# Optimization experiments

Measured on AMD Instinct MI355X. Metric: run time of the kernel, lower is better.

The kernel has to match this reference:

```python
import jax, jax.numpy as jnp
import numpy as np


def setup_inputs() -> dict:
    key = jax.random.key(0)
    k1, k2, k3 = jax.random.split(key, 3)
    B, N, F = 32, 1024, 128
    x = jax.random.normal(k1, (B, N, F), dtype=jnp.float32)
    adj = jax.random.uniform(k2, (B, N, N), dtype=jnp.float32)
    # Linear(in_feature=128, out_feature=128) params (Kaiming-ish scale)
    W = jax.random.normal(k3, (F, F), dtype=jnp.float32) * (1.0 / np.sqrt(F))
    b = jnp.zeros((F,), dtype=jnp.float32)
    return {"x": x, "adj": adj, "W": W, "b": b}


def reference(x, adj, W, b):
    # h = W(x) ; dropout is identity in inference mode
    h = jnp.einsum("bnf,fg->bng", x, W) + b          # [B,N,F]
    h = jnp.einsum("bnm,bmf->bnf", adj, h)           # neighbor aggregation
    return jax.nn.relu(h + x)                          # residual + ReLU
```

## Files before the change

kernel.cpp:

```cpp
#include <hip/hip_runtime.h>
#include <stdint.h>

typedef unsigned short u16;
typedef __attribute__((ext_vector_type(4))) u16    u16x4;
typedef __attribute__((ext_vector_type(8))) u16    u16x8;
typedef __attribute__((ext_vector_type(4))) float  f32x4;
typedef __attribute__((ext_vector_type(8))) __bf16 bf16x8;

__device__ __forceinline__ u16 f2bf(float f) {
    union { float f; uint32_t u; } v; v.f = f;
    uint32_t u = v.u;
    uint32_t rb = 0x7FFFu + ((u >> 16) & 1u);
    return (u16)((u + rb) >> 16);
}

__global__ __launch_bounds__(256) void gcn_wt(const float* __restrict__ W,
                                              u16* __restrict__ Wt) {
    int idx = blockIdx.x * 256 + threadIdx.x;
    int k = idx >> 7, f = idx & 127;
    Wt[f * 128 + k] = f2bf(W[idx]);
}

__global__ __launch_bounds__(512, 4) void gcn_fused(const float* __restrict__ adj,
                                                    const float* __restrict__ x,
                                                    const u16* __restrict__ Wt,
                                                    const float* __restrict__ bias,
                                                    float* __restrict__ out) {
    __shared__ u16   Al[2][64 * 64];
    __shared__ u16   Xt[2][128 * 72];
    __shared__ u16   Yl[64 * 128];
    __shared__ float Rs[64];

    const int t = threadIdx.x;
    const int L  = (blockIdx.x & 7) * 64 + (blockIdx.x >> 3);
    const int bb = L >> 4;
    const int r0 = (L & 15) << 6;

    const float* adjb = adj + (size_t)bb * 1048576 + (size_t)r0 * 1024;
    const float* xb   = x + (size_t)bb * 131072;

    const int w = t >> 6, l = t & 63;
    const int wr = w >> 1, wc = w & 1;

    const int rA = t >> 3, k8 = t & 7;
    const float* gA = adjb + (size_t)rA * 1024 + k8 * 8;
    const int ldsA = rA * 128 + ((k8 * 16) ^ ((rA & 7) << 4));

    const float* gX = xb + (size_t)wr * 128 + wc * 64 + l;
    const int xWb = (wc * 64 + l) * 144 + 2 * wr;

    float rsum = 0.0f;

#define LOADT(ar, xr, ks)                                       \
    do {                                                        \
        const int n0_ = (ks) * 64;                              \
        ar[0] = *(const f32x4*)(gA + n0_);                      \
        ar[1] = *(const f32x4*)(gA + n0_ + 4);                  \
        _Pragma("unroll")                                       \
        for (int i = 0; i < 16; ++i)                            \
            xr[i] = gX[(size_t)n0_ * 128 + i * 512];            \
    } while (0)

#define WRITET(buf, ar, xr)                                     \
    do {                                                        \
        u16x8 ha;                                               \
        ha[0] = f2bf(ar[0].x); ha[1] = f2bf(ar[0].y);           \
        ha[2] = f2bf(ar[0].z); ha[3] = f2bf(ar[0].w);           \
        ha[4] = f2bf(ar[1].x); ha[5] = f2bf(ar[1].y);           \
        ha[6] = f2bf(ar[1].z); ha[7] = f2bf(ar[1].w);           \
        *(u16x8*)((char*)&Al[buf][0] + ldsA) = ha;              \
        rsum += ar[0].x + ar[0].y + ar[0].z + ar[0].w           \
              + ar[1].x + ar[1].y + ar[1].z + ar[1].w;          \
        _Pragma("unroll")                                       \
        for (int i = 0; i < 16; ++i)                            \
            *(u16*)((char*)&Xt[buf][0] + xWb + i * 8) = f2bf(xr[i]); \
    } while (0)

#define BARRIER() asm volatile("s_waitcnt lgkmcnt(0)\ns_barrier" ::: "memory")

#define COMPUTE(buf)                                                            \
    do {                                                                        \
        _Pragma("unroll")                                                       \
        for (int kk = 0; kk < 2; ++kk) {                                        \
            const int kbyteA = kk * 64 + (l >> 4) * 16;                         \
            const int rl = wr * 16 + (l & 15);                                  \
            bf16x8 a = *(const bf16x8*)((const char*)&Al[buf][0] + rl * 128 +   \
                                        (kbyteA ^ ((rl & 7) << 4)));            \
            bf16x8 b[4];                                                        \
            _Pragma("unroll")                                                   \
            for (int nn = 0; nn < 4; ++nn) {                                    \
                int fm = wc * 64 + nn * 16 + (l & 15);                          \
                b[nn] = *(const bf16x8*)((const char*)&Xt[buf][0] + fm * 144 +  \
                                         kk * 64 + (l >> 4) * 16);              \
            }                                                                   \
            _Pragma("unroll")                                                   \
            for (int nn = 0; nn < 4; ++nn)                                      \
                acc[nn] = __builtin_amdgcn_mfma_f32_16x16x32_bf16(              \
                    a, b[nn], acc[nn], 0, 0, 0);                                \
        }                                                                       \
    } while (0)

    f32x4 acc[4] = {};
    f32x4 a0[2], a1[2];
    float xs0[16], xs1[16];

    LOADT(a0, xs0, 0);
    LOADT(a1, xs1, 1);
#pragma unroll
    for (int ks = 0; ks < 16; ks += 2) {
        WRITET(0, a0, xs0);
        BARRIER();
        if (ks + 2 < 16) LOADT(a0, xs0, ks + 2);
        COMPUTE(0);
        WRITET(1, a1, xs1);
        BARRIER();
        if (ks + 3 < 16) LOADT(a1, xs1, ks + 3);
        COMPUTE(1);
    }
#undef LOADT
#undef WRITET
#undef BARRIER
#undef COMPUTE

    rsum += __shfl_xor(rsum, 1);
    rsum += __shfl_xor(rsum, 2);
    rsum += __shfl_xor(rsum, 4);
    if ((t & 7) == 0) Rs[rA] = rsum;

#pragma unroll
    for (int nn = 0; nn < 4; ++nn)
#pragma unroll
        for (int j = 0; j < 4; ++j) {
            int r = wr * 16 + (l >> 4) * 4 + j;
            int c = wc * 64 + nn * 16 + (l & 15);
            *(u16*)((char*)Yl + r * 256 + ((c * 2) ^ ((r & 7) << 4))) =
                f2bf(acc[nn][j]);
        }
    __syncthreads();

    f32x4 z[4] = {};
    const int rl2 = wr * 16 + (l & 15);
#pragma unroll
    for (int kk = 0; kk < 4; ++kk) {
        const int kbyte = kk * 64 + (l >> 4) * 16;
        bf16x8 a = *(const bf16x8*)((const char*)Yl + rl2 * 256 +
                                    (kbyte ^ ((rl2 & 7) << 4)));
#pragma unroll
        for (int nn = 0; nn < 4; ++nn) {
            int f = wc * 64 + nn * 16 + (l & 15);
            int k = kk * 32 + (l >> 4) * 8;
            bf16x8 b = *(const bf16x8*)(Wt + (size_t)f * 128 + k);
            z[nn] = __builtin_amdgcn_mfma_f32_16x16x32_bf16(a, b, z[nn], 0, 0, 0);
        }
    }

    float* ob = out + (size_t)bb * 131072;
#pragma unroll
    for (int nn = 0; nn < 4; ++nn) {
        int f = wc * 64 + nn * 16 + (l & 15);
        float bv = bias[f];
#pragma unroll
        for (int j = 0; j < 4; ++j) {
            int r = wr * 16 + (l >> 4) * 4 + j;
            size_t idx = (size_t)(r0 + r) * 128 + f;
            float v = z[nn][j] + Rs[r] * bv + xb[idx];
            ob[idx] = fmaxf(v, 0.0f);
        }
    }
}

extern "C" void kernel_launch(void* const* d_in, const int* in_sizes, int n_in,
                              void* d_out, int out_size, void* d_ws, size_t ws_size,
                              hipStream_t stream) {
    const float* x    = (const float*)d_in[0];
    const float* adj  = (const float*)d_in[1];
    const float* W    = (const float*)d_in[2];
    const float* bias = (const float*)d_in[3];
    float* out = (float*)d_out;

    u16* Wt = (u16*)d_ws;

    gcn_wt   <<<dim3(64),  dim3(256), 0, stream>>>(W, Wt);
    gcn_fused<<<dim3(512), dim3(512), 0, stream>>>(adj, x, Wt, bias, out);
}
```

Measured before the change: 49.71 us.

## Compute h=xW+b per K-tile inside the main loop, single kernel launch

Replaces the (adj·x)·W ordering with adj·(xW+b): each K-chunk of x is first multiplied by register-resident W fragments (bias folded into the accumulator init), then fed as the B operand of the adj MFMA. This removes the separate W transpose kernel, the row-sum reduction and the second post-loop GEMM through LDS, and reads the residual from the LDS x tile instead of reloading it from global. The cost is recomputing xW per block (16x redundant across row blocks), more MFMA work per K step and extra bf16 rounding of the intermediate h and of the residual x.

After: 42.32 us. 14.9% less time.

```diff
diff --git a/kernel.cpp b/kernel.cpp
--- a/kernel.cpp
+++ b/kernel.cpp
@@ -7,6 +7,9 @@
 typedef __attribute__((ext_vector_type(4))) float  f32x4;
 typedef __attribute__((ext_vector_type(8))) __bf16 bf16x8;
 
+union BF8 { u16x8 u; bf16x8 b; };
+union BF4x2 { struct { u16x4 lo, hi; } p; bf16x8 b; };
+
 __device__ __forceinline__ u16 f2bf(float f) {
     union { float f; uint32_t u; } v; v.f = f;
     uint32_t u = v.u;
@@ -14,159 +17,172 @@
     return (u16)((u + rb) >> 16);
 }
 
-__global__ __launch_bounds__(256) void gcn_wt(const float* __restrict__ W,
-                                              u16* __restrict__ Wt) {
-    int idx = blockIdx.x * 256 + threadIdx.x;
-    int k = idx >> 7, f = idx & 127;
-    Wt[f * 128 + k] = f2bf(W[idx]);
-}
-
-__global__ __launch_bounds__(512, 4) void gcn_fused(const float* __restrict__ adj,
-                                                    const float* __restrict__ x,
-                                                    const u16* __restrict__ Wt,
-                                                    const float* __restrict__ bias,
-                                                    float* __restrict__ out) {
-    __shared__ u16   Al[2][64 * 64];
-    __shared__ u16   Xt[2][128 * 72];
-    __shared__ u16   Yl[64 * 128];
-    __shared__ float Rs[64];
+__global__ __launch_bounds__(512, 4) void gcn_one(const float* __restrict__ adj,
+                                                  const float* __restrict__ x,
+                                                  const float* __restrict__ W,
+                                                  const float* __restrict__ bias,
+                                                  float* __restrict__ out) {
+    __shared__ u16 Al[2][64 * 64];
+    __shared__ u16 Xl[2][64 * 128];
+    __shared__ u16 Xr[64 * 128];
 
     const int t = threadIdx.x;
-    const int L  = (blockIdx.x & 7) * 64 + (blockIdx.x >> 3);
+    const int L = (blockIdx.x & 7) * 64 + (blockIdx.x >> 3);
     const int bb = L >> 4;
-    const int r0 = (L & 15) << 6;
+    const int myblk = L & 15;
+    const int r0 = myblk << 6;
 
     const float* adjb = adj + (size_t)bb * 1048576 + (size_t)r0 * 1024;
     const float* xb   = x + (size_t)bb * 131072;
 
     const int w = t >> 6, l = t & 63;
-    const int wr = w >> 1, wc = w & 1;
+    const int lg = l >> 4, lc = l & 15;
+    const int f = w * 16 + lc;
 
-    const int rA = t >> 3, k8 = t & 7;
-    const float* gA = adjb + (size_t)rA * 1024 + k8 * 8;
-    const int ldsA = rA * 128 + ((k8 * 16) ^ ((rA & 7) << 4));
+    const float bv = bias[f];
+    BF8 wf[4];
+#pragma unroll
+    for (int gs = 0; gs < 4; ++gs)
+#pragma unroll
+        for (int j = 0; j < 8; ++j)
+            wf[gs].b[j] = (__bf16)W[(size_t)(gs * 32 + lg * 8 + j) * 128 + f];
 
-    const float* gX = xb + (size_t)wr * 128 + wc * 64 + l;
-    const int xWb = (wc * 64 + l) * 144 + 2 * wr;
+    const int rA0 = t >> 4;
+    const int rA1 = rA0 + 32;
+    const int aOff = (t & 15) * 8;
+    const int ldsA0 = rA0 * 128 + (aOff ^ (((rA0 & 7) << 4) | (rA0 & 8)));
+    const int ldsA1 = rA1 * 128 + (aOff ^ (((rA1 & 7) << 4) | (rA1 & 8)));
+    const float* gA0 = adjb + (size_t)rA0 * 1024 + (t & 15) * 4;
+    const float* gA1 = adjb + (size_t)rA1 * 1024 + (t & 15) * 4;
 
-    float rsum = 0.0f;
+    const int xOff = (t & 31) * 8;
+    int ldsX[4];
+    const float* gX[4];
+#pragma unroll
+    for (int i = 0; i < 4; ++i) {
+        int n = (t >> 5) + i * 16;
+        ldsX[i] = n * 256 + (xOff ^ ((n & 7) << 4));
+        gX[i] = xb + (size_t)n * 128 + (t & 31) * 4;
+    }
 
-#define LOADT(ar, xr, ks)                                       \
-    do {                                                        \
-        const int n0_ = (ks) * 64;                              \
-        ar[0] = *(const f32x4*)(gA + n0_);                      \
-        ar[1] = *(const f32x4*)(gA + n0_ + 4);                  \
-        _Pragma("unroll")                                       \
-        for (int i = 0; i < 16; ++i)                            \
-            xr[i] = gX[(size_t)n0_ * 128 + i * 512];            \
+#define LOADT(ar, xr, ks)                                         \
+    do {                                                          \
+        ar[0] = *(const f32x4*)(gA0 + (ks) * 64);                 \
+        ar[1] = *(const f32x4*)(gA1 + (ks) * 64);                 \
+        _Pragma("unroll")                                         \
+        for (int i = 0; i < 4; ++i)                               \
+            xr[i] = *(const f32x4*)(gX[i] + (size_t)(ks) * 8192); \
     } while (0)
 
-#define WRITET(buf, ar, xr)                                     \
-    do {                                                        \
-        u16x8 ha;                                               \
-        ha[0] = f2bf(ar[0].x); ha[1] = f2bf(ar[0].y);           \
-        ha[2] = f2bf(ar[0].z); ha[3] = f2bf(ar[0].w);           \
-        ha[4] = f2bf(ar[1].x); ha[5] = f2bf(ar[1].y);           \
-        ha[6] = f2bf(ar[1].z); ha[7] = f2bf(ar[1].w);           \
-        *(u16x8*)((char*)&Al[buf][0] + ldsA) = ha;              \
-        rsum += ar[0].x + ar[0].y + ar[0].z + ar[0].w           \
-              + ar[1].x + ar[1].y + ar[1].z + ar[1].w;          \
-        _Pragma("unroll")                                       \
-        for (int i = 0; i < 16; ++i)                            \
-            *(u16*)((char*)&Xt[buf][0] + xWb + i * 8) = f2bf(xr[i]); \
+#define WRITET(buf, ar, xr)                                              \
+    do {                                                                 \
+        u16x4 h0, h1;                                                    \
+        h0.x = f2bf(ar[0].x); h0.y = f2bf(ar[0].y);                      \
+        h0.z = f2bf(ar[0].z); h0.w = f2bf(ar[0].w);                      \
+        h1.x = f2bf(ar[1].x); h1.y = f2bf(ar[1].y);                      \
+        h1.z = f2bf(ar[1].z); h1.w = f2bf(ar[1].w);                      \
+        *(u16x4*)((char*)&Al[buf][0] + ldsA0) = h0;                      \
+        *(u16x4*)((char*)&Al[buf][0] + ldsA1) = h1;                      \
+        _Pragma("unroll")                                                \
+        for (int i = 0; i < 4; ++i) {                                    \
+            u16x4 hx;                                                    \
+            hx.x = f2bf(xr[i].x); hx.y = f2bf(xr[i].y);                  \
+            hx.z = f2bf(xr[i].z); hx.w = f2bf(xr[i].w);                  \
+            *(u16x4*)((char*)&Xl[buf][0] + ldsX[i]) = hx;                \
+        }                                                                \
     } while (0)
 
 #define BARRIER() asm volatile("s_waitcnt lgkmcnt(0)\ns_barrier" ::: "memory")
 
-#define COMPUTE(buf)                                                            \
-    do {                                                                        \
-        _Pragma("unroll")                                                       \
-        for (int kk = 0; kk < 2; ++kk) {                                        \
-            const int kbyteA = kk * 64 + (l >> 4) * 16;                         \
-            const int rl = wr * 16 + (l & 15);                                  \
-            bf16x8 a = *(const bf16x8*)((const char*)&Al[buf][0] + rl * 128 +   \
-                                        (kbyteA ^ ((rl & 7) << 4)));            \
-            bf16x8 b[4];                                                        \
-            _Pragma("unroll")                                                   \
-            for (int nn = 0; nn < 4; ++nn) {                                    \
-                int fm = wc * 64 + nn * 16 + (l & 15);                          \
-                b[nn] = *(const bf16x8*)((const char*)&Xt[buf][0] + fm * 144 +  \
-                                         kk * 64 + (l >> 4) * 16);              \
-            }                                                                   \
-            _Pragma("unroll")                                                   \
-            for (int nn = 0; nn < 4; ++nn)                                      \
-                acc[nn] = __builtin_amdgcn_mfma_f32_16x16x32_bf16(              \
-                    a, b[nn], acc[nn], 0, 0, 0);                                \
-        }                                                                       \
+#define COPYRESID(buf)                                                        \
+    do {                                                                      \
+        u16x8 c0 = *(const u16x8*)((const char*)&Xl[buf][0] + t * 32);        \
+        u16x8 c1 = *(const u16x8*)((const char*)&Xl[buf][0] + t * 32 + 16);   \
+        *(u16x8*)((char*)Xr + t * 32)      = c0;                              \
+        *(u16x8*)((char*)Xr + t * 32 + 16) = c1;                              \
     } while (0)
 
-    f32x4 acc[4] = {};
-    f32x4 a0[2], a1[2];
-    float xs0[16], xs1[16];
+#define COMPUTE(buf)                                                               \
+    do {                                                                           \
+        f32x4 hacc[4];                                                             \
+        _Pragma("unroll")                                                          \
+        for (int nb = 0; nb < 4; ++nb) {                                           \
+            f32x4 hv = {bv, bv, bv, bv};                                           \
+            hacc[nb] = hv;                                                         \
+        }                                                                          \
+        _Pragma("unroll")                                                          \
+        for (int gs = 0; gs < 4; ++gs) {                                           \
+            _Pragma("unroll")                                                      \
+            for (int nb = 0; nb < 4; ++nb) {                                       \
+                int n = nb * 16 + lc;                                              \
+                BF8 xa;                                                            \
+                xa.u = *(const u16x8*)((const char*)&Xl[buf][0] + n * 256 +        \
+                                       ((gs * 64 + lg * 16) ^ ((n & 7) << 4)));    \
+                hacc[nb] = __builtin_amdgcn_mfma_f32_16x16x32_bf16(                \
+                    xa.b, wf[gs].b, hacc[nb], 0, 0, 0);                            \
+            }                                                                      \
+        }                                                                          \
+        BF8 hb0, hb1;                                                              \
+        hb0.b[0] = (__bf16)hacc[0].x; hb0.b[1] = (__bf16)hacc[0].y;                \
+        hb0.b[2] = (__bf16)hacc[0].z; hb0.b[3] = (__bf16)hacc[0].w;                \
+        hb0.b[4] = (__bf16)hacc[1].x; hb0.b[5] = (__bf16)hacc[1].y;                \
+        hb0.b[6] = (__bf16)hacc[1].z; hb0.b[7] = (__bf16)hacc[1].w;                \
+        hb1.b[0] = (__bf16)hacc[2].x; hb1.b[1] = (__bf16)hacc[2].y;                \
+        hb1.b[2] = (__bf16)hacc[2].z; hb1.b[3] = (__bf16)hacc[2].w;                \
+        hb1.b[4] = (__bf16)hacc[3].x; hb1.b[5] = (__bf16)hacc[3].y;                \
+        hb1.b[6] = (__bf16)hacc[3].z; hb1.b[7] = (__bf16)hacc[3].w;                \
+        _Pragma("unroll")                                                          \
+        for (int kn = 0; kn < 2; ++kn) {                                           \
+            _Pragma("unroll")                                                      \
+            for (int rb = 0; rb < 4; ++rb) {                                       \
+                int r = rb * 16 + lc;                                              \
+                int msk = ((r & 7) << 4) | (r & 8);                                \
+                BF4x2 af;                                                          \
+                af.p.lo = *(const u16x4*)((const char*)&Al[buf][0] + r * 128 +     \
+                                          ((kn * 64 + lg * 8) ^ msk));             \
+                af.p.hi = *(const u16x4*)((const char*)&Al[buf][0] + r * 128 +     \
+                                          ((kn * 64 + 32 + lg * 8) ^ msk));        \
+                yacc[rb] = __builtin_amdgcn_mfma_f32_16x16x32_bf16(                \
+                    af.b, (kn ? hb1.b : hb0.b), yacc[rb], 0, 0, 0);                \
+            }                                                                      \
+        }                                                                          \
+    } while (0)
 
-    LOADT(a0, xs0, 0);
-    LOADT(a1, xs1, 1);
+    f32x4 yacc[4] = {};
+    f32x4 ar[2];
+    f32x4 xr[4];
+
+    LOADT(ar, xr, 0);
 #pragma unroll
-    for (int ks = 0; ks < 16; ks += 2) {
-        WRITET(0, a0, xs0);
+    for (int ks = 0; ks < 16; ++ks) {
+        const int buf = ks & 1;
+        WRITET(buf, ar, xr);
         BARRIER();
-        if (ks + 2 < 16) LOADT(a0, xs0, ks + 2);
-        COMPUTE(0);
-        WRITET(1, a1, xs1);
-        BARRIER();
-        if (ks + 3 < 16) LOADT(a1, xs1, ks + 3);
-        COMPUTE(1);
+        if (ks + 1 < 16) LOADT(ar, xr, ks + 1);
+        if (ks == myblk) COPYRESID(buf);
+        COMPUTE(buf);
     }
 #undef LOADT
 #undef WRITET
 #undef BARRIER
+#undef COPYRESID
 #undef COMPUTE
 
-    rsum += __shfl_xor(rsum, 1);
-    rsum += __shfl_xor(rsum, 2);
-    rsum += __shfl_xor(rsum, 4);
-    if ((t & 7) == 0) Rs[rA] = rsum;
+    __syncthreads();
 
+    float* ob = out + (size_t)bb * 131072 + (size_t)r0 * 128;
 #pragma unroll
-    for (int nn = 0; nn < 4; ++nn)
+    for (int rb = 0; rb < 4; ++rb)
 #pragma unroll
         for (int j = 0; j < 4; ++j) {
-            int r = wr * 16 + (l >> 4) * 4 + j;
-            int c = wc * 64 + nn * 16 + (l & 15);
-            *(u16*)((char*)Yl + r * 256 + ((c * 2) ^ ((r & 7) << 4))) =
-                f2bf(acc[nn][j]);
+            int rr = rb * 16 + lg * 4 + j;
+            u16 xv = *(const u16*)((const char*)Xr + rr * 256 +
+                                   ((f * 2) ^ ((rr & 7) << 4)));
+            union { float ff; uint32_t uu; } cv;
+            cv.uu = (uint32_t)xv << 16;
+            float v = yacc[rb][j] + cv.ff;
+            ob[(size_t)rr * 128 + f] = fmaxf(v, 0.0f);
         }
-    __syncthreads();
-
-    f32x4 z[4] = {};
-    const int rl2 = wr * 16 + (l & 15);
-#pragma unroll
-    for (int kk = 0; kk < 4; ++kk) {
-        const int kbyte = kk * 64 + (l >> 4) * 16;
-        bf16x8 a = *(const bf16x8*)((const char*)Yl + rl2 * 256 +
-                                    (kbyte ^ ((rl2 & 7) << 4)));
-#pragma unroll
-        for (int nn = 0; nn < 4; ++nn) {
-            int f = wc * 64 + nn * 16 + (l & 15);
-            int k = kk * 32 + (l >> 4) * 8;
-            bf16x8 b = *(const bf16x8*)(Wt + (size_t)f * 128 + k);
-            z[nn] = __builtin_amdgcn_mfma_f32_16x16x32_bf16(a, b, z[nn], 0, 0, 0);
-        }
-    }
-
-    float* ob = out + (size_t)bb * 131072;
-#pragma unroll
-    for (int nn = 0; nn < 4; ++nn) {
-        int f = wc * 64 + nn * 16 + (l & 15);
-        float bv = bias[f];
-#pragma unroll
-        for (int j = 0; j < 4; ++j) {
-            int r = wr * 16 + (l >> 4) * 4 + j;
-            size_t idx = (size_t)(r0 + r) * 128 + f;
-            float v = z[nn][j] + Rs[r] * bv + xb[idx];
-            ob[idx] = fmaxf(v, 0.0f);
-        }
-    }
 }
 
 extern "C" void kernel_launch(void* const* d_in, const int* in_sizes, int n_in,
@@ -178,8 +194,5 @@
     const float* bias = (const float*)d_in[3];
     float* out = (float*)d_out;
 
-    u16* Wt = (u16*)d_ws;
-
-    gcn_wt   <<<dim3(64),  dim3(256), 0, stream>>>(W, Wt);
-    gcn_fused<<<dim3(512), dim3(512), 0, stream>>>(adj, x, Wt, bias, out);
+    gcn_one<<<dim3(512), dim3(512), 0, stream>>>(adj, x, W, bias, out);
 }
```
